# Performance work log

Measured on AMD Instinct MI355X. Metric: run time of the kernel, lower is better.

Reference implementation:

```python
import jax, jax.numpy as jnp
import numpy as np

HEADS = 16
DIM_HEAD = 64


def setup_inputs() -> dict:
    key = jax.random.key(0)
    k1, k2, k3, k4, k5 = jax.random.split(key, 5)
    B, S, E = 4, 2048, 1024
    inner = HEADS * DIM_HEAD  # 1024
    return {
        "hidden_states": jax.random.normal(k1, (B, S, E), dtype=jnp.float32),
        "w_q": jax.random.normal(k2, (E, inner), dtype=jnp.float32) * (E ** -0.5),
        "w_k": jax.random.normal(k3, (E, inner), dtype=jnp.float32) * (E ** -0.5),
        "w_v": jax.random.normal(k4, (E, inner), dtype=jnp.float32) * (E ** -0.5),
        "w_o": jax.random.normal(k5, (inner, E), dtype=jnp.float32) * (inner ** -0.5),
    }


def reference(hidden_states, w_q, w_k, w_v, w_o):
    # Self-attention path: context = hidden_states (context arg is None).
    B, S, _ = hidden_states.shape
    dtype = hidden_states.dtype
    scale = DIM_HEAD ** -0.5

    q = (hidden_states @ w_q).reshape(B, S, HEADS, DIM_HEAD)
    k = (hidden_states @ w_k).reshape(B, S, HEADS, DIM_HEAD)
    v = (hidden_states @ w_v).reshape(B, S, HEADS, DIM_HEAD)

    # fp32 softmax as in the original module
    q32 = q.astype(jnp.float32)
    k32 = k.astype(jnp.float32)
    scores = jnp.einsum('btnh,bfnh->bnft', k32, q32) * scale  # [B, H, S_q, S_kv]
    probs = jax.nn.softmax(scores, axis=-1).astype(dtype)

    out = jnp.einsum('bnft,btnh->bfnh', probs, v)  # [B, S, H, D]
    out = out.reshape(B, S, HEADS * DIM_HEAD)
    return out @ w_o  # [B, S, query_dim]
```

## Files before the change

kernel.cpp:

```cpp
#include <hip/hip_runtime.h>
#include <stdint.h>

typedef __attribute__((ext_vector_type(8))) unsigned short ushort8;
typedef __attribute__((ext_vector_type(8))) __bf16 bf16x8;
typedef __attribute__((ext_vector_type(4))) float f32x4;
typedef __attribute__((ext_vector_type(4))) uint32_t u32x4;

#define TBK 32

__device__ __forceinline__ unsigned short f2bf(float f) {
  union { float f; uint32_t u; } x; x.f = f;
  uint32_t u = x.u;
  uint32_t r = (u + 0x7fffu + ((u >> 16) & 1u)) >> 16;
  return (unsigned short)r;
}

__device__ __forceinline__ uint32_t pack_bf2(float lo, float hi) {
  return (uint32_t)f2bf(lo) | ((uint32_t)f2bf(hi) << 16);
}

__device__ __forceinline__ uint32_t rhu2(float lo, float hi) {
  union { float f; uint32_t u; } a, b; a.f = lo; b.f = hi;
  return __builtin_amdgcn_perm(b.u + 0x8000u, a.u + 0x8000u, 0x07060302u);
}

__device__ __forceinline__ void store_c(unsigned short* p, float v) { *p = f2bf(v); }
__device__ __forceinline__ void store_c(float* p, float v) { *p = v; }

__device__ __forceinline__ void gll16(const unsigned short* g, unsigned short* l) {
  __builtin_amdgcn_global_load_lds((const __attribute__((address_space(1))) void*)g,
                                   (__attribute__((address_space(3))) void*)l,
                                   16, 0, 0);
}

__global__ __launch_bounds__(256) void cvt_f32_bf16(
    const float* __restrict__ x, unsigned short* __restrict__ y, int n4) {
  int i = blockIdx.x * 256 + threadIdx.x;
  if (i >= n4) return;
  float4 v = *(const float4*)(x + (size_t)i * 4);
  uint2 p; p.x = pack_bf2(v.x, v.y); p.y = pack_bf2(v.z, v.w);
  *(uint2*)(y + (size_t)i * 4) = p;
}

__global__ void transpose_w(const float* __restrict__ W,
                            unsigned short* __restrict__ WT) {
  __shared__ unsigned short tile[32][33];
  int c0 = blockIdx.x * 32, r0 = blockIdx.y * 32;
  int x = threadIdx.x, y = threadIdx.y;
#pragma unroll
  for (int i = 0; i < 32; i += 8)
    tile[y + i][x] = f2bf(W[(size_t)(r0 + y + i) * 1024 + c0 + x]);
  __syncthreads();
#pragma unroll
  for (int i = 0; i < 32; i += 8)
    WT[(size_t)(c0 + y + i) * 1024 + r0 + x] = tile[x][y + i];
}

template <typename OutT>
__global__ __launch_bounds__(256) void gemm_bt(
    const unsigned short* A,
    const unsigned short* BT0, const unsigned short* BT1, const unsigned short* BT2,
    OutT* C0, OutT* C1, OutT* C2,
    int M, int N, int K) {
  const unsigned short* BT = (blockIdx.z == 0) ? BT0 : (blockIdx.z == 1) ? BT1 : BT2;
  OutT* C = (blockIdx.z == 0) ? C0 : (blockIdx.z == 1) ? C1 : C2;

  __shared__ __attribute__((aligned(16))) unsigned short As[128 * TBK];
  __shared__ __attribute__((aligned(16))) unsigned short Bs[128 * TBK];

  const int tid = threadIdx.x;
  const int wave = tid >> 6, lane = tid & 63;
  const int fr = lane & 15, fq = lane >> 4;
  const int bm = blockIdx.x * 128, bn = blockIdx.y * 128;
  const int wm = (wave >> 1) * 64, wn = (wave & 1) * 64;

  f32x4 acc[4][4] = {};

  const int sr = lane >> 2;
  const int sk = (lane & 3) * 8;
  const unsigned short* Ag = A + (size_t)(bm + wave * 32 + sr) * K + sk;
  const unsigned short* Bg = BT + (size_t)(bn + wave * 32 + sr) * K + sk;
  unsigned short* As0 = &As[(wave * 32) * TBK];
  unsigned short* Bs0 = &Bs[(wave * 32) * TBK];

  for (int k0 = 0; k0 < K; k0 += TBK) {
    gll16(Ag + k0, As0);
    gll16(Ag + k0 + 16 * K, As0 + 16 * TBK);
    gll16(Bg + k0, Bs0);
    gll16(Bg + k0 + 16 * K, Bs0 + 16 * TBK);
    asm volatile("s_waitcnt vmcnt(0)" ::: "memory");
    __syncthreads();

    bf16x8 af[4], bfr[4];
#pragma unroll
    for (int mt = 0; mt < 4; mt++)
      af[mt] = *(const bf16x8*)&As[(wm + mt * 16 + fr) * TBK + fq * 8];
#pragma unroll
    for (int nt = 0; nt < 4; nt++)
      bfr[nt] = *(const bf16x8*)&Bs[(wn + nt * 16 + fr) * TBK + fq * 8];
#pragma unroll
    for (int mt = 0; mt < 4; mt++)
#pragma unroll
      for (int nt = 0; nt < 4; nt++)
        acc[mt][nt] = __builtin_amdgcn_mfma_f32_16x16x32_bf16(af[mt], bfr[nt], acc[mt][nt], 0, 0, 0);
    __syncthreads();
  }

#pragma unroll
  for (int mt = 0; mt < 4; mt++)
#pragma unroll
    for (int nt = 0; nt < 4; nt++)
#pragma unroll
      for (int r = 0; r < 4; r++) {
        int row = bm + wm + mt * 16 + fq * 4 + r;
        int col = bn + wn + nt * 16 + fr;
        store_c(&C[(size_t)row * N + col], acc[mt][nt][r]);
      }
}

#define SQ 72

__global__ __launch_bounds__(256) void attn_kernel(
    const unsigned short* q, const unsigned short* k,
    const unsigned short* v, unsigned short* o) {
  const int S = 2048, E = 1024;
  __shared__ __attribute__((aligned(16))) unsigned short Ks[64 * SQ];
  __shared__ __attribute__((aligned(16))) unsigned short Vt[64 * SQ];

  const int tid = threadIdx.x;
  const int wave = tid >> 6, lane = tid & 63;
  const int fr = lane & 15, fq = lane >> 4;
  const int q0 = blockIdx.x * 64;
  const int bh = blockIdx.y;
  const int b = bh >> 4, h = bh & 15;
  const size_t base = ((size_t)b * S) * E + (size_t)h * 64;

  bf16x8 aq[2];
#pragma unroll
  for (int ks = 0; ks < 2; ks++)
    aq[ks] = *(const bf16x8*)&q[base + (size_t)(q0 + wave * 16 + fr) * E + ks * 32 + fq * 8];

  ushort8 ones_u;
#pragma unroll
  for (int j = 0; j < 8; j++) ones_u[j] = 0x3F80;
  bf16x8 onesf = *(bf16x8*)&ones_u;

  f32x4 ot[4] = {};
  f32x4 osum = {};
  const float KSC = 0.125f * 1.44269504088896341f;

  const int rp = (tid & 31) * 2;
  const int dcv = (tid >> 5) * 8;
  const int u_ = rp & 31;
  const int slot = 32 * (rp >> 5) + 8 * ((u_ & 15) >> 2) + 4 * (u_ >> 4) + (u_ & 3);

  for (int t0 = 0; t0 < S; t0 += 64) {
    __syncthreads();
#pragma unroll
    for (int i = 0; i < 2; i++) {
      int id = tid + i * 256;
      int row = id >> 3, dc = (id & 7) * 8;
      ushort8 kv = *(const ushort8*)&k[base + (size_t)(t0 + row) * E + dc];
      *(ushort8*)&Ks[row * SQ + dc] = kv;
    }
    {
      u32x4 a = *(const u32x4*)&v[base + (size_t)(t0 + rp) * E + dcv];
      u32x4 bb = *(const u32x4*)&v[base + (size_t)(t0 + rp + 1) * E + dcv];
#pragma unroll
      for (int w = 0; w < 4; w++) {
        uint32_t lo = __builtin_amdgcn_perm(bb[w], a[w], 0x05040100u);
        uint32_t hi = __builtin_amdgcn_perm(bb[w], a[w], 0x07060302u);
        *(uint32_t*)&Vt[(dcv + 2 * w) * SQ + slot] = lo;
        *(uint32_t*)&Vt[(dcv + 2 * w + 1) * SQ + slot] = hi;
      }
    }
    __syncthreads();

    f32x4 st[4] = {};
#pragma unroll
    for (int ks = 0; ks < 2; ks++) {
#pragma unroll
      for (int tt = 0; tt < 4; tt++) {
        bf16x8 ak = *(const bf16x8*)&Ks[(tt * 16 + fr) * SQ + ks * 32 + fq * 8];
        st[tt] = __builtin_amdgcn_mfma_f32_16x16x32_bf16(ak, aq[ks], st[tt], 0, 0, 0);
      }
    }

    uint32_t pk[4][2];
#pragma unroll
    for (int tt = 0; tt < 4; tt++) {
      float e0 = __builtin_amdgcn_exp2f(st[tt][0] * KSC);
      float e1 = __builtin_amdgcn_exp2f(st[tt][1] * KSC);
      float e2 = __builtin_amdgcn_exp2f(st[tt][2] * KSC);
      float e3 = __builtin_amdgcn_exp2f(st[tt][3] * KSC);
      pk[tt][0] = rhu2(e0, e1);
      pk[tt][1] = rhu2(e2, e3);
    }

#pragma unroll
    for (int c = 0; c < 2; c++) {
      u32x4 bpr;
      bpr[0] = pk[2 * c][0];
      bpr[1] = pk[2 * c][1];
      bpr[2] = pk[2 * c + 1][0];
      bpr[3] = pk[2 * c + 1][1];
      bf16x8 bp = *(bf16x8*)&bpr;
#pragma unroll
      for (int dt = 0; dt < 4; dt++) {
        bf16x8 av = *(const bf16x8*)&Vt[(dt * 16 + fr) * SQ + c * 32 + fq * 8];
        ot[dt] = __builtin_amdgcn_mfma_f32_16x16x32_bf16(av, bp, ot[dt], 0, 0, 0);
      }
      osum = __builtin_amdgcn_mfma_f32_16x16x32_bf16(onesf, bp, osum, 0, 0, 0);
    }
  }

  {
    float inv = 1.0f / osum[0];
    size_t rowbase = base + (size_t)(q0 + wave * 16 + fr) * E;
#pragma unroll
    for (int dt = 0; dt < 4; dt++) {
      uint32_t w0 = rhu2(ot[dt][0] * inv, ot[dt][1] * inv);
      uint32_t w1 = rhu2(ot[dt][2] * inv, ot[dt][3] * inv);
      *(uint32_t*)&o[rowbase + dt * 16 + fq * 4] = w0;
      *(uint32_t*)&o[rowbase + dt * 16 + fq * 4 + 2] = w1;
    }
  }
}

extern "C" void kernel_launch(void* const* d_in, const int* in_sizes, int n_in,
                              void* d_out, int out_size, void* d_ws, size_t ws_size,
                              hipStream_t stream) {
  const float* hs = (const float*)d_in[0];
  const float* wq = (const float*)d_in[1];
  const float* wk = (const float*)d_in[2];
  const float* wv = (const float*)d_in[3];
  const float* wo = (const float*)d_in[4];
  unsigned short* ws = (unsigned short*)d_ws;

  unsigned short* wqT = ws;
  unsigned short* wkT = ws + 1048576;
  unsigned short* wvT = ws + 2097152;
  unsigned short* woT = wqT;
  unsigned short* qb  = ws + 3145728;
  unsigned short* kb  = qb + 8388608;
  unsigned short* vb  = kb + 8388608;
  unsigned short* ob  = qb;
  unsigned short* hsb = (unsigned short*)d_out;
  float* out = (float*)d_out;

  const int M = 8192, N = 1024, K = 1024;

  cvt_f32_bf16<<<dim3(M * K / 4 / 256), 256, 0, stream>>>(hs, hsb, M * K / 4);

  dim3 tb(32, 8);
  transpose_w<<<dim3(32, 32), tb, 0, stream>>>(wq, wqT);
  transpose_w<<<dim3(32, 32), tb, 0, stream>>>(wk, wkT);
  transpose_w<<<dim3(32, 32), tb, 0, stream>>>(wv, wvT);

  gemm_bt<unsigned short><<<dim3(M / 128, N / 128, 3), 256, 0, stream>>>(
      hsb, wqT, wkT, wvT, qb, kb, vb, M, N, K);

  transpose_w<<<dim3(32, 32), tb, 0, stream>>>(wo, woT);

  attn_kernel<<<dim3(2048 / 64, 64), 256, 0, stream>>>(qb, kb, vb, ob);

  gemm_bt<float><<<dim3(M / 128, N / 128, 1), 256, 0, stream>>>(
      ob, woT, woT, woT, out, out, out, M, N, K);
}
```

Measured before the change: 304.7 us.

## Process two query groups per attention block to reuse K/V tiles

Each attention block now covers 128 query rows instead of 64. Every wave keeps two sets of Q fragments and accumulators, so each K/V tile staged in shared memory feeds twice as many MFMAs. This halves K/V global loads and LDS staging per query and gives the scheduler more independent MFMAs. The costs are twice the accumulator registers, a launch-bounds hint of 4 blocks per SM, and half as many blocks (1024).

Result: faster. 289.6 us (-4.9%).

```diff
diff --git a/kernel.cpp b/kernel.cpp
--- a/kernel.cpp
+++ b/kernel.cpp
@@ -120,7 +120,7 @@
 
 #define SQ 72
 
-__global__ __launch_bounds__(256) void attn_kernel(
+__global__ __launch_bounds__(256, 4) void attn_kernel(
     const unsigned short* q, const unsigned short* k,
     const unsigned short* v, unsigned short* o) {
   const int S = 2048, E = 1024;
@@ -130,23 +130,26 @@
   const int tid = threadIdx.x;
   const int wave = tid >> 6, lane = tid & 63;
   const int fr = lane & 15, fq = lane >> 4;
-  const int q0 = blockIdx.x * 64;
+  const int q0 = blockIdx.x * 128;
   const int bh = blockIdx.y;
   const int b = bh >> 4, h = bh & 15;
   const size_t base = ((size_t)b * S) * E + (size_t)h * 64;
 
-  bf16x8 aq[2];
-#pragma unroll
-  for (int ks = 0; ks < 2; ks++)
-    aq[ks] = *(const bf16x8*)&q[base + (size_t)(q0 + wave * 16 + fr) * E + ks * 32 + fq * 8];
+  bf16x8 aq[2][2];
+#pragma unroll
+  for (int qg = 0; qg < 2; qg++)
+#pragma unroll
+    for (int ks = 0; ks < 2; ks++)
+      aq[qg][ks] = *(const bf16x8*)&q[base +
+          (size_t)(q0 + qg * 64 + wave * 16 + fr) * E + ks * 32 + fq * 8];
 
   ushort8 ones_u;
 #pragma unroll
   for (int j = 0; j < 8; j++) ones_u[j] = 0x3F80;
   bf16x8 onesf = *(bf16x8*)&ones_u;
 
-  f32x4 ot[4] = {};
-  f32x4 osum = {};
+  f32x4 ot[2][4] = {};
+  f32x4 osum[2] = {};
   const float KSC = 0.125f * 1.44269504088896341f;
 
   const int rp = (tid & 31) * 2;
@@ -176,51 +179,61 @@
     }
     __syncthreads();
 
-    f32x4 st[4] = {};
+    f32x4 st[2][4] = {};
 #pragma unroll
     for (int ks = 0; ks < 2; ks++) {
 #pragma unroll
       for (int tt = 0; tt < 4; tt++) {
         bf16x8 ak = *(const bf16x8*)&Ks[(tt * 16 + fr) * SQ + ks * 32 + fq * 8];
-        st[tt] = __builtin_amdgcn_mfma_f32_16x16x32_bf16(ak, aq[ks], st[tt], 0, 0, 0);
-      }
-    }
-
-    uint32_t pk[4][2];
-#pragma unroll
-    for (int tt = 0; tt < 4; tt++) {
-      float e0 = __builtin_amdgcn_exp2f(st[tt][0] * KSC);
-      float e1 = __builtin_amdgcn_exp2f(st[tt][1] * KSC);
-      float e2 = __builtin_amdgcn_exp2f(st[tt][2] * KSC);
-      float e3 = __builtin_amdgcn_exp2f(st[tt][3] * KSC);
-      pk[tt][0] = rhu2(e0, e1);
-      pk[tt][1] = rhu2(e2, e3);
-    }
+        st[0][tt] = __builtin_amdgcn_mfma_f32_16x16x32_bf16(ak, aq[0][ks], st[0][tt], 0, 0, 0);
+        st[1][tt] = __builtin_amdgcn_mfma_f32_16x16x32_bf16(ak, aq[1][ks], st[1][tt], 0, 0, 0);
+      }
+    }
+
+    uint32_t pk[2][4][2];
+#pragma unroll
+    for (int qg = 0; qg < 2; qg++)
+#pragma unroll
+      for (int tt = 0; tt < 4; tt++) {
+        float e0 = __builtin_amdgcn_exp2f(st[qg][tt][0] * KSC);
+        float e1 = __builtin_amdgcn_exp2f(st[qg][tt][1] * KSC);
+        float e2 = __builtin_amdgcn_exp2f(st[qg][tt][2] * KSC);
+        float e3 = __builtin_amdgcn_exp2f(st[qg][tt][3] * KSC);
+        pk[qg][tt][0] = rhu2(e0, e1);
+        pk[qg][tt][1] = rhu2(e2, e3);
+      }
 
 #pragma unroll
     for (int c = 0; c < 2; c++) {
-      u32x4 bpr;
-      bpr[0] = pk[2 * c][0];
-      bpr[1] = pk[2 * c][1];
-      bpr[2] = pk[2 * c + 1][0];
-      bpr[3] = pk[2 * c + 1][1];
-      bf16x8 bp = *(bf16x8*)&bpr;
+      bf16x8 bp[2];
+#pragma unroll
+      for (int qg = 0; qg < 2; qg++) {
+        u32x4 bpr;
+        bpr[0] = pk[qg][2 * c][0];
+        bpr[1] = pk[qg][2 * c][1];
+        bpr[2] = pk[qg][2 * c + 1][0];
+        bpr[3] = pk[qg][2 * c + 1][1];
+        bp[qg] = *(bf16x8*)&bpr;
+      }
 #pragma unroll
       for (int dt = 0; dt < 4; dt++) {
         bf16x8 av = *(const bf16x8*)&Vt[(dt * 16 + fr) * SQ + c * 32 + fq * 8];
-        ot[dt] = __builtin_amdgcn_mfma_f32_16x16x32_bf16(av, bp, ot[dt], 0, 0, 0);
-      }
-      osum = __builtin_amdgcn_mfma_f32_16x16x32_bf16(onesf, bp, osum, 0, 0, 0);
+        ot[0][dt] = __builtin_amdgcn_mfma_f32_16x16x32_bf16(av, bp[0], ot[0][dt], 0, 0, 0);
+        ot[1][dt] = __builtin_amdgcn_mfma_f32_16x16x32_bf16(av, bp[1], ot[1][dt], 0, 0, 0);
+      }
+      osum[0] = __builtin_amdgcn_mfma_f32_16x16x32_bf16(onesf, bp[0], osum[0], 0, 0, 0);
+      osum[1] = __builtin_amdgcn_mfma_f32_16x16x32_bf16(onesf, bp[1], osum[1], 0, 0, 0);
     }
   }
 
-  {
-    float inv = 1.0f / osum[0];
-    size_t rowbase = base + (size_t)(q0 + wave * 16 + fr) * E;
+#pragma unroll
+  for (int qg = 0; qg < 2; qg++) {
+    float inv = 1.0f / osum[qg][0];
+    size_t rowbase = base + (size_t)(q0 + qg * 64 + wave * 16 + fr) * E;
 #pragma unroll
     for (int dt = 0; dt < 4; dt++) {
-      uint32_t w0 = rhu2(ot[dt][0] * inv, ot[dt][1] * inv);
-      uint32_t w1 = rhu2(ot[dt][2] * inv, ot[dt][3] * inv);
+      uint32_t w0 = rhu2(ot[qg][dt][0] * inv, ot[qg][dt][1] * inv);
+      uint32_t w1 = rhu2(ot[qg][dt][2] * inv, ot[qg][dt][3] * inv);
       *(uint32_t*)&o[rowbase + dt * 16 + fq * 4] = w0;
       *(uint32_t*)&o[rowbase + dt * 16 + fq * 4 + 2] = w1;
     }
@@ -262,7 +275,7 @@
 
   transpose_w<<<dim3(32, 32), tb, 0, stream>>>(wo, woT);
 
-  attn_kernel<<<dim3(2048 / 64, 64), 256, 0, stream>>>(qb, kb, vb, ob);
+  attn_kernel<<<dim3(2048 / 128, 64), 256, 0, stream>>>(qb, kb, vb, ob);
 
   gemm_bt<float><<<dim3(M / 128, N / 128, 1), 256, 0, stream>>>(
       ob, woT, woT, woT, out, out, out, M, N, K);
```
